# Performance work log

Hardware: AMD Instinct MI355X
Metric: run time of the kernel (lower is better)

## Reference

```python
import jax, jax.numpy as jnp
import numpy as np

N_NODES = 100000
N_EDGES = 1600000
IN_CH = 128
OUT_CH = 128
N_REL = 64
N_BASES = 8


def setup_inputs() -> dict:
    key = jax.random.key(0)
    k = jax.random.split(key, 7)
    x = jax.random.normal(k[0], (N_NODES, IN_CH), dtype=jnp.float32)
    src = jax.random.randint(k[1], (N_EDGES,), 0, N_NODES, dtype=jnp.int32)
    rel = jax.random.randint(k[2], (N_EDGES,), 0, N_REL, dtype=jnp.int32)
    dst = jax.random.randint(k[3], (N_EDGES,), 0, N_NODES, dtype=jnp.int32)
    edge_triples = jnp.stack([src, rel, dst], axis=1)  # [E, 3] (src, rel, dst)
    # xavier-uniform-ish scales
    basis = jax.random.normal(k[4], (N_BASES, IN_CH, OUT_CH), dtype=jnp.float32) * (2.0 / (IN_CH + OUT_CH)) ** 0.5
    att = jax.random.normal(k[5], (N_REL, N_BASES), dtype=jnp.float32) * (2.0 / (N_REL + N_BASES)) ** 0.5
    root_w = jax.random.normal(k[6], (IN_CH, OUT_CH), dtype=jnp.float32) * (1.0 / IN_CH) ** 0.5
    root_b = jnp.zeros((OUT_CH,), dtype=jnp.float32)
    return {"x": x, "edge_triples": edge_triples, "num_nodes": N_NODES,
            "basis": basis, "att": att, "root_w": root_w, "root_b": root_b}


def reference(x, edge_triples, num_nodes, basis, att, root_w, root_b):
    src = edge_triples[:, 0]
    rel = edge_triples[:, 1]
    dst = edge_triples[:, 2]
    att_e = att[rel]  # [E, B]
    n_bases = basis.shape[0]
    e = src.shape[0]
    out_ch = basis.shape[2]
    # messages[e] = x[src[e]] @ (sum_b att[rel[e], b] * basis[b])
    # computed as sum_b att_e[:, b] * (x @ basis[b])[src] to avoid the huge
    # per-edge [E, in, out] weight gather the torch code materializes.
    msgs = jnp.zeros((e, out_ch), dtype=x.dtype)
    for b in range(n_bases):  # small fixed loop over bases
        yb = x @ basis[b]  # [N, out]
        msgs = msgs + att_e[:, b:b + 1] * yb[src]
    # degree normalization (mean aggregation over incoming edges)
    deg = jax.ops.segment_sum(jnp.ones((e,), dtype=x.dtype), dst, num_segments=num_nodes)
    deg_inv = jnp.where(deg > 0, 1.0 / deg, 0.0)
    msgs = msgs * deg_inv[dst][:, None]
    agg = jax.ops.segment_sum(msgs, dst, num_segments=num_nodes)  # [N, out]
    return agg + x @ root_w + root_b
```

## Files before the change

### kernel.cpp

```cpp
#include <hip/hip_runtime.h>

#define NCH 128
#define NREL 64
#define NBP 1024
#define ESB 4096
#define CAPF 3072
#define CAPH 2048
#define KTOT 1152
#define KST 36
#define ZROW 2304

typedef __attribute__((ext_vector_type(8))) short bf16x8;
typedef __attribute__((ext_vector_type(4))) float f32x4;

__device__ __forceinline__ unsigned short f2bf(float f) {
    unsigned u = __float_as_uint(f);
    return (unsigned short)((u + 0x7fffu + ((u >> 16) & 1u)) >> 16);
}
__device__ __forceinline__ unsigned pack2bf(float a, float b) {
    return (unsigned)f2bf(a) | ((unsigned)f2bf(b) << 16);
}

__global__ __launch_bounds__(256) void k_prep(const float* __restrict__ x,
                                              unsigned short* __restrict__ x_bf,
                                              long total8) {
    long i = (long)blockIdx.x * 256 + threadIdx.x;
    if (i >= total8) return;
    const float4* xp = (const float4*)x;
    float4 v0 = xp[i * 2], v1 = xp[i * 2 + 1];
    bf16x8 p;
    p[0] = (short)f2bf(v0.x); p[1] = (short)f2bf(v0.y);
    p[2] = (short)f2bf(v0.z); p[3] = (short)f2bf(v0.w);
    p[4] = (short)f2bf(v1.x); p[5] = (short)f2bf(v1.y);
    p[6] = (short)f2bf(v1.z); p[7] = (short)f2bf(v1.w);
    ((bf16x8*)x_bf)[i] = p;
}

__global__ __launch_bounds__(256) void k_buildB(const float* __restrict__ basis,
                                                const float* __restrict__ att,
                                                const float* __restrict__ rw,
                                                unsigned short* __restrict__ attB,
                                                unsigned short* __restrict__ basisP) {
    int idx = blockIdx.x * 256 + threadIdx.x;
    if (idx < 1040) {
        int rr = idx >> 4, b = idx & 15;
        attB[idx] = (rr < NREL && b < 8) ? f2bf(att[rr * 8 + b]) : (unsigned short)0;
    }
    if (idx >= 128 * KTOT) return;
    int j = idx & 7, lg = (idx >> 3) & 3, oc = (idx >> 5) & 127, kk = idx >> 12;
    int k = kk * 32 + lg * 8 + j;
    float v;
    if (k < 1024) {
        int b = k & 7, ch = k >> 3;
        v = basis[(size_t)b * NCH * NCH + (size_t)ch * NCH + oc];
    } else {
        v = rw[(size_t)(k - 1024) * NCH + oc];
    }
    basisP[idx] = f2bf(v);
}

__global__ __launch_bounds__(256) void k_count(const int* __restrict__ trip, int E, int NB,
                                               int* __restrict__ cntB) {
    __shared__ int hb[NBP];
    int t = threadIdx.x;
    for (int i = t; i < NB; i += 256) hb[i] = 0;
    __syncthreads();
    int base = blockIdx.x * ESB;
#pragma unroll
    for (int i = 0; i < ESB / 256; ++i) {
        int e = base + i * 256 + t;
        if (e < E) atomicAdd(&hb[trip[3 * e + 2] >> 7], 1);
    }
    __syncthreads();
    for (int i = t; i < NB; i += 256) cntB[(size_t)blockIdx.x * NB + i] = hb[i];
}

__global__ __launch_bounds__(1024) void k_scanB(int* __restrict__ cntB, int GB, int NB,
                                                int* __restrict__ bhist) {
    __shared__ int sc[1024];
    int t = threadIdx.x, b = blockIdx.x;
    int v = (t < GB) ? cntB[(size_t)t * NB + b] : 0;
    sc[t] = v;
    __syncthreads();
    for (int off = 1; off < 1024; off <<= 1) {
        int a = (t >= off) ? sc[t - off] : 0;
        __syncthreads();
        sc[t] += a;
        __syncthreads();
    }
    if (t < GB) cntB[(size_t)t * NB + b] = sc[t] - v;
    if (t == GB - 1) bhist[b] = sc[t];
}

__global__ __launch_bounds__(1024) void k_offsets(const int* __restrict__ bhist, int NB,
                                                  int* __restrict__ bucketoff) {
    __shared__ int sc[1024];
    int t = threadIdx.x;
    int d = (t < NB) ? bhist[t] : 0;
    sc[t] = d;
    __syncthreads();
    for (int off = 1; off < 1024; off <<= 1) {
        int a = (t >= off) ? sc[t - off] : 0;
        __syncthreads();
        sc[t] += a;
        __syncthreads();
    }
    if (t < NB) bucketoff[t] = sc[t] - d;
    if (t == NB - 1) bucketoff[NB] = sc[t];
}

__global__ __launch_bounds__(256) void k_scatter(const int* __restrict__ trip, int E, int NB,
                                                 const int* __restrict__ cntB,
                                                 const int* __restrict__ bucketoff,
                                                 unsigned* __restrict__ packed) {
    __shared__ int cb[NBP], lbase[NBP], delta[NBP];
    __shared__ int ssc[256];
    __shared__ unsigned lpk[ESB];
    __shared__ unsigned short lb[ESB];
    int t = threadIdx.x, blk = blockIdx.x;
    for (int i = t; i < NB; i += 256) cb[i] = 0;
    __syncthreads();
    int base = blk * ESB;
    int total = min(ESB, E - base);

    unsigned pk[ESB / 256];
    int rk[ESB / 256];
    unsigned short bk[ESB / 256];
#pragma unroll
    for (int i = 0; i < ESB / 256; ++i) {
        int e = base + i * 256 + t;
        pk[i] = 0; rk[i] = 0; bk[i] = 0;
        if (e < E) {
            int src = trip[3 * e], rel = trip[3 * e + 1], dst = trip[3 * e + 2];
            int bkt = dst >> 7;
            bk[i] = (unsigned short)bkt;
            pk[i] = ((unsigned)(dst & 127) << 23) | ((unsigned)rel << 17) | (unsigned)src;
            rk[i] = atomicAdd(&cb[bkt], 1);
        }
    }
    __syncthreads();
    int ch = (NB + 255) >> 8;
    int mysum = 0;
    for (int i = 0; i < ch; ++i) {
        int idx = t * ch + i;
        if (idx < NB) mysum += cb[idx];
    }
    ssc[t] = mysum;
    __syncthreads();
    for (int off = 1; off < 256; off <<= 1) {
        int a = (t >= off) ? ssc[t - off] : 0;
        __syncthreads();
        ssc[t] += a;
        __syncthreads();
    }
    int run = ssc[t] - mysum;
    for (int i = 0; i < ch; ++i) {
        int idx = t * ch + i;
        if (idx < NB) { lbase[idx] = run; run += cb[idx]; }
    }
    __syncthreads();
    for (int i = t; i < NB; i += 256)
        delta[i] = bucketoff[i] + cntB[(size_t)blk * NB + i] - lbase[i];
    __syncthreads();
#pragma unroll
    for (int i = 0; i < ESB / 256; ++i) {
        int e = base + i * 256 + t;
        if (e < E) {
            int j = lbase[bk[i]] + rk[i];
            lpk[j] = pk[i];
            lb[j] = bk[i];
        }
    }
    __syncthreads();
    for (int j = t; j < total; j += 256)
        packed[delta[lb[j]] + j] = lpk[j];
}

__global__ __launch_bounds__(256) void k_sortbkt(const unsigned* __restrict__ packed,
                                                 const int* __restrict__ bucketoff,
                                                 unsigned* __restrict__ sortedG,
                                                 int* __restrict__ dstoffG) {
    __shared__ int h[128], hs[128];
    int t = threadIdx.x, b = blockIdx.x;
    if (t < 128) h[t] = 0;
    __syncthreads();
    int s0 = bucketoff[b], s1 = bucketoff[b + 1];
    int cnt = min(s1 - s0, CAPF);

    unsigned pk[CAPF / 256];
    int rk[CAPF / 256];
#pragma unroll
    for (int i = 0; i < CAPF / 256; ++i) {
        int j = i * 256 + t;
        pk[i] = 0; rk[i] = 0;
        if (j < cnt) {
            unsigned p = packed[s0 + j];
            pk[i] = p;
            rk[i] = atomicAdd(&h[p >> 23], 1);
        }
    }
    __syncthreads();
    if (t < 128) hs[t] = h[t];
    __syncthreads();
    for (int off = 1; off < 128; off <<= 1) {
        int a = (t < 128 && t >= off) ? hs[t - off] : 0;
        __syncthreads();
        if (t < 128) hs[t] += a;
        __syncthreads();
    }
    if (t < 128) dstoffG[b * 129 + t] = hs[t] - h[t];
    if (t == 0) dstoffG[b * 129 + 128] = cnt;
#pragma unroll
    for (int i = 0; i < CAPF / 256; ++i) {
        int j = i * 256 + t;
        if (j < cnt) {
            int d = pk[i] >> 23;
            sortedG[s0 + hs[d] - h[d] + rk[i]] = pk[i];
        }
    }
}

__global__ __launch_bounds__(512, 4) void k_fused(const unsigned* __restrict__ x32,
                                                  const unsigned short* __restrict__ xus,
                                                  const unsigned* __restrict__ sortedG,
                                                  const int* __restrict__ bucketoff,
                                                  const int* __restrict__ dstoffG,
                                                  const unsigned short* __restrict__ attBg,
                                                  const unsigned short* __restrict__ basisP,
                                                  const float* __restrict__ rb,
                                                  float* __restrict__ out, int N) {
    __shared__ bf16x8 ztV[16 * (ZROW / 16)];
    __shared__ unsigned sortedE[CAPH];
    __shared__ unsigned short attl[1056];
    __shared__ int doffsL[65];
    __shared__ int nextD;
    char* zt = (char*)ztV;

    int t = threadIdx.x;
    int bucket = blockIdx.x >> 1, half = blockIdx.x & 1;
    int w = t >> 6, lane = t & 63, lr = lane & 15, lg = lane >> 4;
    int l15 = lane & 15;
    int nb0 = bucket * 128 + half * 64;

    for (int i = t; i < 1040; i += 512) attl[i] = attBg[i];
    int rawIdx = bucket * 129 + half * 64;
    int rawBase = dstoffG[rawIdx];
    int cnt = min(dstoffG[rawIdx + 64] - rawBase, CAPH);
    if (t < 65) doffsL[t] = min(dstoffG[rawIdx + t] - rawBase, CAPH);
    if (t == 0) nextD = 0;
    int sG0 = bucketoff[bucket] + rawBase;
    for (int j = t; j < cnt; j += 512) {
        unsigned p = sortedG[sG0 + j];
        sortedE[j] = (((p >> 17) & 63u) << 26) | ((p & 0x1FFFFu) << 8);
    }
    __syncthreads();

    for (int r = 0; r < 4; ++r) {
        int rEnd = r * 16 + 16;

        for (;;) {
            int my = 0x7FFFFFFF;
            if (lane == 0) my = atomicAdd(&nextD, 1);
            my = __shfl(my, 0, 64);
            if (my >= rEnd) break;
            int d = my;
            int eBeg = doffsL[d], eEnd = doffsL[d + 1];
            int cnt_d = eEnd - eBeg;
            int n = nb0 + d;
            unsigned xv = (n < N) ? x32[(size_t)n * 64 + lane] : 0u;

            f32x4 acc[8];
#pragma unroll
            for (int nt = 0; nt < 8; ++nt) acc[nt] = (f32x4){0.f, 0.f, 0.f, 0.f};

            int last = eEnd - 1;
            for (int c0 = eBeg; c0 < eEnd; c0 += 32) {
                int kb = c0 + (lg << 3);
                bf16x8 aF;
                bf16x8 bF[8];
#pragma unroll
                for (int j = 0; j < 8; ++j) {
                    int e = kb + j;
                    unsigned ew = sortedE[min(e, last)];
                    int arow = (e < eEnd) ? (int)(ew >> 26) : 64;
                    aF[j] = (short)attl[arow * 16 + l15];
                    unsigned xi = ((ew & 0x03FFFF00u) >> 1) + (unsigned)l15;
                    bF[0][j] = (short)xus[xi];
                    bF[1][j] = (short)xus[xi + 16];
                    bF[2][j] = (short)xus[xi + 32];
                    bF[3][j] = (short)xus[xi + 48];
                    bF[4][j] = (short)xus[xi + 64];
                    bF[5][j] = (short)xus[xi + 80];
                    bF[6][j] = (short)xus[xi + 96];
                    bF[7][j] = (short)xus[xi + 112];
                }
#pragma unroll
                for (int nt = 0; nt < 8; ++nt)
                    acc[nt] = __builtin_amdgcn_mfma_f32_16x16x32_bf16(aF, bF[nt], acc[nt], 0, 0, 0);
            }

            float inv = (cnt_d > 0) ? 1.f / (float)cnt_d : 0.f;
            int zr = d & 15, sw = zr & 7;
            char* zrow = zt + zr * ZROW;
            if (lane < 32) {
                int b0 = (lane >> 4) << 2;
#pragma unroll
                for (int nt = 0; nt < 8; ++nt) {
                    int chn = nt * 16 + l15;
                    uint2 v;
                    v.x = pack2bf(acc[nt][0] * inv, acc[nt][1] * inv);
                    v.y = pack2bf(acc[nt][2] * inv, acc[nt][3] * inv);
                    *(uint2*)(zrow + ((chn ^ sw) << 4) + (b0 << 1)) = v;
                }
            }
            *(unsigned*)(zrow + (((128 + (lane >> 2)) ^ sw) << 4) + ((lane & 3) << 2)) = xv;
        }
        __syncthreads();

        f32x4 accM = {0.f, 0.f, 0.f, 0.f};
        int ocr = w * 16 + lr;
        int swm = lr & 7;
#pragma unroll 6
        for (int kk = 0; kk < KST; ++kk) {
            bf16x8 a = *(const bf16x8*)(zt + lr * ZROW + ((((kk << 2) + lg) ^ swm) << 4));
            bf16x8 b0 = *(const bf16x8*)(basisP + ((((size_t)kk * 128 + ocr) * 4 + lg) << 3));
            accM = __builtin_amdgcn_mfma_f32_16x16x32_bf16(b0, a, accM, 0, 0, 0);
        }

        int n = nb0 + r * 16 + lr;
        if (n < N) {
            int oc0 = w * 16 + lg * 4;
            f32x4 bias = *(const f32x4*)(rb + oc0);
            *(f32x4*)(out + (size_t)n * NCH + oc0) = accM + bias;
        }
        if (t == 0) nextD = rEnd;
        __syncthreads();
    }
}

extern "C" void kernel_launch(void* const* d_in, const int* in_sizes, int n_in,
                              void* d_out, int out_size, void* d_ws, size_t ws_size,
                              hipStream_t stream) {
    const float* x = (const float*)d_in[0];
    const int* trip = (const int*)d_in[1];
    const float* basis = (const float*)d_in[3];
    const float* att = (const float*)d_in[4];
    const float* rw = (const float*)d_in[5];
    const float* rb = (const float*)d_in[6];
    float* out = (float*)d_out;

    int N = in_sizes[0] / NCH;
    int E = in_sizes[1] / 3;
    int NB = (N + 127) >> 7;
    int GB = (E + ESB - 1) / ESB;

    char* ws = (char*)d_ws;
    size_t off = 0;
    auto alloc = [&](size_t bts) { size_t o = off; off = (off + bts + 255) & ~(size_t)255; return o; };
    size_t oXbf    = alloc((size_t)N * NCH * 2);
    size_t oBasisP = alloc((size_t)128 * KTOT * 2);
    size_t oAttB   = alloc(1056 * 2);
    size_t oCntB   = alloc((size_t)GB * NB * 4);
    size_t oBhist  = alloc((NBP + 1) * 4);
    size_t oBktoff = alloc((NBP + 1) * 4);
    size_t oPacked = alloc((size_t)E * 4);
    size_t oSorted = alloc((size_t)E * 4);
    size_t oDoff   = alloc((size_t)NB * 129 * 4);
    (void)off; (void)ws_size;

    unsigned short* x_bf = (unsigned short*)(ws + oXbf);
    unsigned short* basisP = (unsigned short*)(ws + oBasisP);
    unsigned short* attB = (unsigned short*)(ws + oAttB);
    int* cntB = (int*)(ws + oCntB);
    int* bhist = (int*)(ws + oBhist);
    int* bucketoff = (int*)(ws + oBktoff);
    unsigned* packed = (unsigned*)(ws + oPacked);
    unsigned* sortedG = (unsigned*)(ws + oSorted);
    int* dstoffG = (int*)(ws + oDoff);

    long total8 = (long)N * NCH / 8;
    k_prep<<<(int)((total8 + 255) / 256), 256, 0, stream>>>(x, x_bf, total8);
    k_buildB<<<(128 * KTOT + 255) / 256, 256, 0, stream>>>(basis, att, rw, attB, basisP);
    k_count<<<GB, 256, 0, stream>>>(trip, E, NB, cntB);
    k_scanB<<<NB, 1024, 0, stream>>>(cntB, GB, NB, bhist);
    k_offsets<<<1, 1024, 0, stream>>>(bhist, NB, bucketoff);
    k_scatter<<<GB, 256, 0, stream>>>(trip, E, NB, cntB, bucketoff, packed);
    k_sortbkt<<<NB, 256, 0, stream>>>(packed, bucketoff, sortedG, dstoffG);
    k_fused<<<NB * 2, 512, 0, stream>>>((const unsigned*)x_bf, x_bf, sortedG, bucketoff,
                                        dstoffG, attB, basisP, rb, out, N);
}
```

Measured before the change: 278.9 us.

## Store bf16 x in swizzled layout so gathers use 16-byte vector loads

The bf16 copy of x is written in a permuted layout in which each 16-byte chunk holds the eight channels a lane needs across the eight output tiles. The gather in the fused kernel then does one 128-bit load per edge instead of eight 2-byte loads, and byte-permute instructions rebuild the MFMA B fragments. Because the root-term x row read from the same buffer is now permuted, the root weight rows are reordered to match. The cost is extra permute instructions and a strided read pattern in the prep kernel.

```diff
diff --git a/kernel.cpp b/kernel.cpp
--- a/kernel.cpp
+++ b/kernel.cpp
@@ -22,18 +22,16 @@
 }
 
 __global__ __launch_bounds__(256) void k_prep(const float* __restrict__ x,
-                                              unsigned short* __restrict__ x_bf,
-                                              long total8) {
-    long i = (long)blockIdx.x * 256 + threadIdx.x;
-    if (i >= total8) return;
-    const float4* xp = (const float4*)x;
-    float4 v0 = xp[i * 2], v1 = xp[i * 2 + 1];
+                                              unsigned short* __restrict__ xsw,
+                                              int N) {
+    int idx = blockIdx.x * 256 + threadIdx.x;
+    if (idx >= N * 16) return;
+    int n = idx >> 4, l15 = idx & 15;
+    const float* xr = x + (size_t)n * NCH + l15;
     bf16x8 p;
-    p[0] = (short)f2bf(v0.x); p[1] = (short)f2bf(v0.y);
-    p[2] = (short)f2bf(v0.z); p[3] = (short)f2bf(v0.w);
-    p[4] = (short)f2bf(v1.x); p[5] = (short)f2bf(v1.y);
-    p[6] = (short)f2bf(v1.z); p[7] = (short)f2bf(v1.w);
-    ((bf16x8*)x_bf)[i] = p;
+#pragma unroll
+    for (int nt = 0; nt < 8; ++nt) p[nt] = (short)f2bf(xr[nt * 16]);
+    *(bf16x8*)(xsw + (size_t)n * NCH + l15 * 8) = p;
 }
 
 __global__ __launch_bounds__(256) void k_buildB(const float* __restrict__ basis,
@@ -54,7 +52,9 @@
         int b = k & 7, ch = k >> 3;
         v = basis[(size_t)b * NCH * NCH + (size_t)ch * NCH + oc];
     } else {
-        v = rw[(size_t)(k - 1024) * NCH + oc];
+        int kp = k - 1024;
+        int ic = ((kp & 7) << 4) | (kp >> 3);
+        v = rw[(size_t)ic * NCH + oc];
     }
     basisP[idx] = f2bf(v);
 }
@@ -221,7 +221,7 @@
 }
 
 __global__ __launch_bounds__(512, 4) void k_fused(const unsigned* __restrict__ x32,
-                                                  const unsigned short* __restrict__ xus,
+                                                  const char* __restrict__ xswb,
                                                   const unsigned* __restrict__ sortedG,
                                                   const int* __restrict__ bucketoff,
                                                   const int* __restrict__ dstoffG,
@@ -255,6 +255,8 @@
     }
     __syncthreads();
 
+    const char* xl = xswb + (l15 << 4);
+
     for (int r = 0; r < 4; ++r) {
         int rEnd = r * 16 + 16;
 
@@ -277,26 +279,50 @@
             for (int c0 = eBeg; c0 < eEnd; c0 += 32) {
                 int kb = c0 + (lg << 3);
                 bf16x8 aF;
-                bf16x8 bF[8];
-#pragma unroll
-                for (int j = 0; j < 8; ++j) {
+                unsigned bw[8][4];
+                uint4 vv[4];
+#pragma unroll
+                for (int j = 0; j < 4; ++j) {
                     int e = kb + j;
                     unsigned ew = sortedE[min(e, last)];
                     int arow = (e < eEnd) ? (int)(ew >> 26) : 64;
                     aF[j] = (short)attl[arow * 16 + l15];
-                    unsigned xi = ((ew & 0x03FFFF00u) >> 1) + (unsigned)l15;
-                    bF[0][j] = (short)xus[xi];
-                    bF[1][j] = (short)xus[xi + 16];
-                    bF[2][j] = (short)xus[xi + 32];
-                    bF[3][j] = (short)xus[xi + 48];
-                    bF[4][j] = (short)xus[xi + 64];
-                    bF[5][j] = (short)xus[xi + 80];
-                    bF[6][j] = (short)xus[xi + 96];
-                    bF[7][j] = (short)xus[xi + 112];
+                    vv[j] = *(const uint4*)(xl + (ew & 0x03FFFF00u));
                 }
 #pragma unroll
+                for (int nt = 0; nt < 8; ++nt) {
+                    unsigned sel = (nt & 1) ? 0x03020706u : 0x01000504u;
+                    int h = nt >> 1;
+                    const unsigned* v0 = (const unsigned*)&vv[0];
+                    const unsigned* v1 = (const unsigned*)&vv[1];
+                    const unsigned* v2 = (const unsigned*)&vv[2];
+                    const unsigned* v3 = (const unsigned*)&vv[3];
+                    bw[nt][0] = __builtin_amdgcn_perm(v0[h], v1[h], sel);
+                    bw[nt][1] = __builtin_amdgcn_perm(v2[h], v3[h], sel);
+                }
+#pragma unroll
+                for (int j = 0; j < 4; ++j) {
+                    int e = kb + 4 + j;
+                    unsigned ew = sortedE[min(e, last)];
+                    int arow = (e < eEnd) ? (int)(ew >> 26) : 64;
+                    aF[4 + j] = (short)attl[arow * 16 + l15];
+                    vv[j] = *(const uint4*)(xl + (ew & 0x03FFFF00u));
+                }
+#pragma unroll
+                for (int nt = 0; nt < 8; ++nt) {
+                    unsigned sel = (nt & 1) ? 0x03020706u : 0x01000504u;
+                    int h = nt >> 1;
+                    const unsigned* v0 = (const unsigned*)&vv[0];
+                    const unsigned* v1 = (const unsigned*)&vv[1];
+                    const unsigned* v2 = (const unsigned*)&vv[2];
+                    const unsigned* v3 = (const unsigned*)&vv[3];
+                    bw[nt][2] = __builtin_amdgcn_perm(v0[h], v1[h], sel);
+                    bw[nt][3] = __builtin_amdgcn_perm(v2[h], v3[h], sel);
+                }
+#pragma unroll
                 for (int nt = 0; nt < 8; ++nt)
-                    acc[nt] = __builtin_amdgcn_mfma_f32_16x16x32_bf16(aF, bF[nt], acc[nt], 0, 0, 0);
+                    acc[nt] = __builtin_amdgcn_mfma_f32_16x16x32_bf16(
+                        aF, *(const bf16x8*)&bw[nt][0], acc[nt], 0, 0, 0);
             }
 
             float inv = (cnt_d > 0) ? 1.f / (float)cnt_d : 0.f;
@@ -368,7 +394,7 @@
     size_t oDoff   = alloc((size_t)NB * 129 * 4);
     (void)off; (void)ws_size;
 
-    unsigned short* x_bf = (unsigned short*)(ws + oXbf);
+    unsigned short* x_sw = (unsigned short*)(ws + oXbf);
     unsigned short* basisP = (unsigned short*)(ws + oBasisP);
     unsigned short* attB = (unsigned short*)(ws + oAttB);
     int* cntB = (int*)(ws + oCntB);
@@ -378,14 +404,13 @@
     unsigned* sortedG = (unsigned*)(ws + oSorted);
     int* dstoffG = (int*)(ws + oDoff);
 
-    long total8 = (long)N * NCH / 8;
-    k_prep<<<(int)((total8 + 255) / 256), 256, 0, stream>>>(x, x_bf, total8);
+    k_prep<<<(N * 16 + 255) / 256, 256, 0, stream>>>(x, x_sw, N);
     k_buildB<<<(128 * KTOT + 255) / 256, 256, 0, stream>>>(basis, att, rw, attB, basisP);
     k_count<<<GB, 256, 0, stream>>>(trip, E, NB, cntB);
     k_scanB<<<NB, 1024, 0, stream>>>(cntB, GB, NB, bhist);
     k_offsets<<<1, 1024, 0, stream>>>(bhist, NB, bucketoff);
     k_scatter<<<GB, 256, 0, stream>>>(trip, E, NB, cntB, bucketoff, packed);
     k_sortbkt<<<NB, 256, 0, stream>>>(packed, bucketoff, sortedG, dstoffG);
-    k_fused<<<NB * 2, 512, 0, stream>>>((const unsigned*)x_bf, x_bf, sortedG, bucketoff,
-                                        dstoffG, attB, basisP, rb, out, N);
-}
+    k_fused<<<NB * 2, 512, 0, stream>>>((const unsigned*)x_sw, (const char*)x_sw, sortedG,
+                                        bucketoff, dstoffG, attB, basisP, rb, out, N);
+}
```

Result: faster. 265.3 us (-4.9%).
